# Optimization experiments

Measured on AMD Instinct MI355X. Metric: run time of the kernel, lower is better.

The kernel has to match this reference:

```python
import jax, jax.numpy as jnp
import numpy as np

EPS = 1e-7
STRIDE = 1
PAD = 3


def _mantissa_map(v):
    # (|v|+eps) * 2^(-floor(log2(|v|+eps))) - 1  -> mantissa-1 in [0,1)
    a = jnp.abs(v) + EPS
    base = a * jnp.exp2(-jnp.floor(jnp.log2(a))) - 1.0
    # piecewise: >=0.5 -> (1+base)/2, else 1+base  (values in [0.75, 1.5))
    return jnp.where(base >= 0.5, (1.0 + base) * 0.5, 1.0 + base)


def _unfold(x, kH, kW, stride, pad, Ho, Wo):
    # im2col matching torch.nn.Unfold ordering (kernel position index = i*kW + j)
    xp = jnp.pad(x, ((0, 0), (0, 0), (pad, pad), (pad, pad)))
    cols = [xp[:, :, i:i + stride * Ho:stride, j:j + stride * Wo:stride]
            for i in range(kH) for j in range(kW)]
    return jnp.stack(cols, axis=-1)  # (B, C, Ho, Wo, kH*kW)


def setup_inputs() -> dict:
    key = jax.random.key(0)
    k1, k2 = jax.random.split(key)
    x = jax.random.normal(k1, (4, 192, 56, 56), dtype=jnp.float32)
    weight = jax.random.normal(k2, (192, 1, 7, 7), dtype=jnp.float32) * 0.1
    return {"x": x, "weight": weight}


def reference(x, weight):
    B, C, H, W = x.shape
    _, _, kH, kW = weight.shape
    Ho = (H + 2 * PAD - kH) // STRIDE + 1
    Wo = (W + 2 * PAD - kW) // STRIDE + 1
    KK = kH * kW

    # mantissa factors
    m2 = _mantissa_map(weight).reshape(C, KK)[None, :, None, None, :]  # (1,C,1,1,KK)
    m1 = _unfold(_mantissa_map(x), kH, kW, STRIDE, PAD, Ho, Wo)        # (B,C,Ho,Wo,KK)
    # zeros come only from unfold's zero padding; map them to 1 (then 0 after -1)
    m1 = jnp.where(m1 == 0.0, 1.0, m1) - 1.0
    m2 = m2 - 1.0

    factor = (m1 + m2 + 1.0) / ((m1 + 1.0) * (m2 + 1.0))
    factor = jnp.where(jnp.isfinite(factor), factor, 1.0)

    q_x = _unfold(x, kH, kW, STRIDE, PAD, Ho, Wo)          # (B,C,Ho,Wo,KK)
    w = weight.reshape(C, KK)[None, :, None, None, :]       # (1,C,1,1,KK)
    q_y = jnp.sum(factor * (q_x * w), axis=-1)              # (B,C,Ho,Wo)
    return q_y.astype(jnp.float32)
```

## Files before the change

### kernel.cpp

```cpp
#include <hip/hip_runtime.h>

typedef float v2f __attribute__((ext_vector_type(2)));
typedef float v4f __attribute__((ext_vector_type(4)));

#define EPS 1e-7f
#define SPW 66

__device__ __forceinline__ float mant_map(float v) {
    float a = fabsf(v) + EPS;
    unsigned int bi = __float_as_uint(a);
    float m = __uint_as_float((bi & 0x007FFFFFu) | 0x3F800000u);
    return (m >= 1.5f) ? 0.5f * m : m;
}

__global__ __launch_bounds__(128, 4) void wconv_kernel(const float* __restrict__ x,
                                                       const float* __restrict__ w,
                                                       float* __restrict__ out) {
    __shared__ v2f sp[14][SPW];
    __shared__ v2f swt[49];

    const int lx = threadIdx.x;
    const int ty = threadIdx.y;
    const int tid = ty * 32 + lx;
    const int c = blockIdx.x;
    const int b = blockIdx.y;
    const int y0 = blockIdx.z * 8;

    const long plane = (long)(b * 192 + c) * 3136;
    const float* xp = x + plane;

    if (tid < 49) {
        float wv = w[c * 49 + tid];
        float M2 = mant_map(wv);
        float B = wv / M2;
        swt[tid] = (v2f){B, B * (M2 - 1.0f)};
    }

    if (tid < 84) {
        int r = tid / 6, k = tid % 6;
        int col = (k < 3) ? k : 56 + k;
        sp[r][col] = (v2f){0.f, 0.f};
    }

    {
        const int t0 = tid, t1 = tid + 128;
        const int r0 = t0 / 14, q0 = t0 % 14;
        const int r1 = t1 / 14, q1 = t1 % 14;
        const int g0 = y0 - 3 + r0, g1 = y0 - 3 + r1;

        v4f u0 = (v4f){0.f, 0.f, 0.f, 0.f}, u1 = u0;
        if (g0 >= 0 && g0 < 56) u0 = *(const v4f*)(xp + g0 * 56 + q0 * 4);
        if (t1 < 196 && g1 >= 0 && g1 < 56) u1 = *(const v4f*)(xp + g1 * 56 + q1 * 4);

        auto stage = [&](int r, int q, v4f u4) {
            v4f* dst = (v4f*)&sp[r][3 + q * 4];
            dst[0] = (v4f){u4.x, u4.x * __builtin_amdgcn_rcpf(mant_map(u4.x)),
                           u4.y, u4.y * __builtin_amdgcn_rcpf(mant_map(u4.y))};
            dst[1] = (v4f){u4.z, u4.z * __builtin_amdgcn_rcpf(mant_map(u4.z)),
                           u4.w, u4.w * __builtin_amdgcn_rcpf(mant_map(u4.w))};
        };
        stage(r0, q0, u0);
        if (t1 < 196) stage(r1, q1, u1);
    }
    __syncthreads();

    {
        const int x0 = ((lx < 28) ? lx : 27) * 2;
        const int rb = ty * 2;

#define LOADROW(P, R)                                                   \
        {                                                               \
            const v4f* s_ = (const v4f*)&sp[(R)][x0];                   \
            v4f t0_ = s_[0], t1_ = s_[1], t2_ = s_[2], t3_ = s_[3];     \
            P[0] = (v2f){t0_.x, t0_.y}; P[1] = (v2f){t0_.z, t0_.w};     \
            P[2] = (v2f){t1_.x, t1_.y}; P[3] = (v2f){t1_.z, t1_.w};     \
            P[4] = (v2f){t2_.x, t2_.y}; P[5] = (v2f){t2_.z, t2_.w};     \
            P[6] = (v2f){t3_.x, t3_.y}; P[7] = (v2f){t3_.z, t3_.w};     \
        }

        v2f RA[8], RB[8];
        LOADROW(RA, rb);
        LOADROW(RB, rb + 1);

        v2f a00 = {0.f, 0.f}, a01 = {0.f, 0.f};
        v2f a10 = {0.f, 0.f}, a11 = {0.f, 0.f};

#define STEP(i, P, Q)                                                   \
        {                                                               \
            _Pragma("unroll")                                           \
            for (int j = 0; j < 7; ++j) {                               \
                v2f wc = swt[(i) * 7 + j];                              \
                a00 += P[j] * wc;  a01 += P[j + 1] * wc;                \
                a10 += Q[j] * wc;  a11 += Q[j + 1] * wc;                \
            }                                                           \
        }

        STEP(0, RA, RB) LOADROW(RA, rb + 2)
        STEP(1, RB, RA) LOADROW(RB, rb + 3)
        STEP(2, RA, RB) LOADROW(RA, rb + 4)
        STEP(3, RB, RA) LOADROW(RB, rb + 5)
        STEP(4, RA, RB) LOADROW(RA, rb + 6)
        STEP(5, RB, RA) LOADROW(RB, rb + 7)
        STEP(6, RA, RB)
#undef STEP
#undef LOADROW

        if (lx < 28) {
            float2 o0 = make_float2(a00.x + a00.y, a01.x + a01.y);
            float2 o1 = make_float2(a10.x + a10.y, a11.x + a11.y);
            *(float2*)&out[plane + (y0 + rb)     * 56 + x0] = o0;
            *(float2*)&out[plane + (y0 + rb + 1) * 56 + x0] = o1;
        }
    }
}

extern "C" void kernel_launch(void* const* d_in, const int* in_sizes, int n_in,
                              void* d_out, int out_size, void* d_ws, size_t ws_size,
                              hipStream_t stream) {
    const float* x = (const float*)d_in[0];
    const float* w = (const float*)d_in[1];
    float* out = (float*)d_out;

    hipLaunchKernelGGL(wconv_kernel, dim3(192, 4, 7), dim3(32, 4), 0, stream, x, w, out);
}
```

Baseline: 71.31 us.

## Compute four output rows per thread with 64-thread blocks and register-cached weights

```diff
diff --git a/kernel.cpp b/kernel.cpp
--- a/kernel.cpp
+++ b/kernel.cpp
@@ -13,9 +13,9 @@
     return (m >= 1.5f) ? 0.5f * m : m;
 }
 
-__global__ __launch_bounds__(128, 4) void wconv_kernel(const float* __restrict__ x,
-                                                       const float* __restrict__ w,
-                                                       float* __restrict__ out) {
+__global__ __launch_bounds__(64, 3) void wconv_kernel(const float* __restrict__ x,
+                                                      const float* __restrict__ w,
+                                                      float* __restrict__ out) {
     __shared__ v2f sp[14][SPW];
     __shared__ v2f swt[49];
 
@@ -36,37 +36,43 @@
         swt[tid] = (v2f){B, B * (M2 - 1.0f)};
     }
 
-    if (tid < 84) {
-        int r = tid / 6, k = tid % 6;
+    for (int t = tid; t < 84; t += 64) {
+        int r = t / 6, k = t % 6;
         int col = (k < 3) ? k : 56 + k;
         sp[r][col] = (v2f){0.f, 0.f};
     }
 
     {
-        const int t0 = tid, t1 = tid + 128;
-        const int r0 = t0 / 14, q0 = t0 % 14;
-        const int r1 = t1 / 14, q1 = t1 % 14;
-        const int g0 = y0 - 3 + r0, g1 = y0 - 3 + r1;
+        const int t0 = tid, t1 = tid + 64, t2 = tid + 128, t3 = tid + 192;
+        const int r0 = t0 / 14, q0 = t0 % 14, g0 = y0 - 3 + r0;
+        const int r1 = t1 / 14, q1 = t1 % 14, g1 = y0 - 3 + r1;
+        const int r2 = t2 / 14, q2 = t2 % 14, g2 = y0 - 3 + r2;
+        const int r3 = t3 / 14, q3 = t3 % 14, g3 = y0 - 3 + r3;
 
-        v4f u0 = (v4f){0.f, 0.f, 0.f, 0.f}, u1 = u0;
+        v4f z4 = (v4f){0.f, 0.f, 0.f, 0.f};
+        v4f u0 = z4, u1 = z4, u2 = z4, u3 = z4;
         if (g0 >= 0 && g0 < 56) u0 = *(const v4f*)(xp + g0 * 56 + q0 * 4);
-        if (t1 < 196 && g1 >= 0 && g1 < 56) u1 = *(const v4f*)(xp + g1 * 56 + q1 * 4);
+        if (g1 >= 0 && g1 < 56) u1 = *(const v4f*)(xp + g1 * 56 + q1 * 4);
+        if (g2 >= 0 && g2 < 56) u2 = *(const v4f*)(xp + g2 * 56 + q2 * 4);
+        if (tid < 4 && g3 >= 0 && g3 < 56) u3 = *(const v4f*)(xp + g3 * 56 + q3 * 4);
 
         auto stage = [&](int r, int q, v4f u4) {
-            v4f* dst = (v4f*)&sp[r][3 + q * 4];
-            dst[0] = (v4f){u4.x, u4.x * __builtin_amdgcn_rcpf(mant_map(u4.x)),
-                           u4.y, u4.y * __builtin_amdgcn_rcpf(mant_map(u4.y))};
-            dst[1] = (v4f){u4.z, u4.z * __builtin_amdgcn_rcpf(mant_map(u4.z)),
-                           u4.w, u4.w * __builtin_amdgcn_rcpf(mant_map(u4.w))};
+            v2f* dst = &sp[r][3 + q * 4];
+            dst[0] = (v2f){u4.x, u4.x * __builtin_amdgcn_rcpf(mant_map(u4.x))};
+            dst[1] = (v2f){u4.y, u4.y * __builtin_amdgcn_rcpf(mant_map(u4.y))};
+            dst[2] = (v2f){u4.z, u4.z * __builtin_amdgcn_rcpf(mant_map(u4.z))};
+            dst[3] = (v2f){u4.w, u4.w * __builtin_amdgcn_rcpf(mant_map(u4.w))};
         };
         stage(r0, q0, u0);
-        if (t1 < 196) stage(r1, q1, u1);
+        stage(r1, q1, u1);
+        stage(r2, q2, u2);
+        if (tid < 4) stage(r3, q3, u3);
     }
     __syncthreads();
 
     {
         const int x0 = ((lx < 28) ? lx : 27) * 2;
-        const int rb = ty * 2;
+        const int rb = ty * 4;
 
 #define LOADROW(P, R)                                                   \
         {                                                               \
@@ -77,39 +83,50 @@
             P[4] = (v2f){t2_.x, t2_.y}; P[5] = (v2f){t2_.z, t2_.w};     \
             P[6] = (v2f){t3_.x, t3_.y}; P[7] = (v2f){t3_.z, t3_.w};     \
         }
-
-        v2f RA[8], RB[8];
-        LOADROW(RA, rb);
-        LOADROW(RB, rb + 1);
-
-        v2f a00 = {0.f, 0.f}, a01 = {0.f, 0.f};
-        v2f a10 = {0.f, 0.f}, a11 = {0.f, 0.f};
-
-#define STEP(i, P, Q)                                                   \
+#define LOADWT(W, I)                                                    \
+        {                                                               \
+            _Pragma("unroll")                                           \
+            for (int j = 0; j < 7; ++j) W[j] = swt[(I) * 7 + j];        \
+        }
+#define PHASE(W, P0, P1, P2, P3)                                        \
         {                                                               \
             _Pragma("unroll")                                           \
             for (int j = 0; j < 7; ++j) {                               \
-                v2f wc = swt[(i) * 7 + j];                              \
-                a00 += P[j] * wc;  a01 += P[j + 1] * wc;                \
-                a10 += Q[j] * wc;  a11 += Q[j + 1] * wc;                \
+                v2f wc = W[j];                                          \
+                a00 += P0[j] * wc;  a01 += P0[j + 1] * wc;              \
+                a10 += P1[j] * wc;  a11 += P1[j + 1] * wc;              \
+                a20 += P2[j] * wc;  a21 += P2[j + 1] * wc;              \
+                a30 += P3[j] * wc;  a31 += P3[j + 1] * wc;              \
             }                                                           \
         }
 
-        STEP(0, RA, RB) LOADROW(RA, rb + 2)
-        STEP(1, RB, RA) LOADROW(RB, rb + 3)
-        STEP(2, RA, RB) LOADROW(RA, rb + 4)
-        STEP(3, RB, RA) LOADROW(RB, rb + 5)
-        STEP(4, RA, RB) LOADROW(RA, rb + 6)
-        STEP(5, RB, RA) LOADROW(RB, rb + 7)
-        STEP(6, RA, RB)
-#undef STEP
+        v2f b0[8], b1[8], b2[8], b3[8];
+        v2f wta[7], wtb[7];
+        v2f a00 = {0.f,0.f}, a01 = {0.f,0.f}, a10 = {0.f,0.f}, a11 = {0.f,0.f};
+        v2f a20 = {0.f,0.f}, a21 = {0.f,0.f}, a30 = {0.f,0.f}, a31 = {0.f,0.f};
+
+        LOADROW(b0, rb + 0) LOADROW(b1, rb + 1) LOADROW(b2, rb + 2) LOADROW(b3, rb + 3)
+        LOADWT(wta, 0)
+        LOADWT(wtb, 1)  PHASE(wta, b0, b1, b2, b3)  LOADROW(b0, rb + 4)
+        LOADWT(wta, 2)  PHASE(wtb, b1, b2, b3, b0)  LOADROW(b1, rb + 5)
+        LOADWT(wtb, 3)  PHASE(wta, b2, b3, b0, b1)  LOADROW(b2, rb + 6)
+        LOADWT(wta, 4)  PHASE(wtb, b3, b0, b1, b2)  LOADROW(b3, rb + 7)
+        LOADWT(wtb, 5)  PHASE(wta, b0, b1, b2, b3)  LOADROW(b0, rb + 8)
+        LOADWT(wta, 6)  PHASE(wtb, b1, b2, b3, b0)  LOADROW(b1, rb + 9)
+                        PHASE(wta, b2, b3, b0, b1)
+#undef PHASE
+#undef LOADWT
 #undef LOADROW
 
         if (lx < 28) {
             float2 o0 = make_float2(a00.x + a00.y, a01.x + a01.y);
             float2 o1 = make_float2(a10.x + a10.y, a11.x + a11.y);
+            float2 o2 = make_float2(a20.x + a20.y, a21.x + a21.y);
+            float2 o3 = make_float2(a30.x + a30.y, a31.x + a31.y);
             *(float2*)&out[plane + (y0 + rb)     * 56 + x0] = o0;
             *(float2*)&out[plane + (y0 + rb + 1) * 56 + x0] = o1;
+            *(float2*)&out[plane + (y0 + rb + 2) * 56 + x0] = o2;
+            *(float2*)&out[plane + (y0 + rb + 3) * 56 + x0] = o3;
         }
     }
 }
@@ -121,5 +138,5 @@
     const float* w = (const float*)d_in[1];
     float* out = (float*)d_out;
 
-    hipLaunchKernelGGL(wconv_kernel, dim3(192, 4, 7), dim3(32, 4), 0, stream, x, w, out);
+    hipLaunchKernelGGL(wconv_kernel, dim3(192, 4, 7), dim3(32, 2), 0, stream, x, w, out);
 }
```

After: 197.8 us. 177% more time.
